# Kernel optimization log

Hardware: AMD Instinct MI355X
Metric: run time of the kernel (lower is better)

## Reference

```python
import jax, jax.numpy as jnp
import numpy as np

IN_C = 256
INTER_C = 64  # in_c // k, k=4
B, H, W = 8, 32, 32
N_TERMS = 5   # numSeriesTerms; numTraceSamples = 1


def setup_inputs():
    key = jax.random.key(0)
    ks = jax.random.split(key, 10)
    s = 0.05
    return {
        "x": jax.random.normal(ks[0], (B, IN_C, H, W), jnp.float32),
        "Wq": jax.random.normal(ks[1], (INTER_C, IN_C), jnp.float32) * s,
        "bq": jax.random.normal(ks[2], (INTER_C,), jnp.float32) * s,
        "Wk": jax.random.normal(ks[3], (INTER_C, IN_C), jnp.float32) * s,
        "bk": jax.random.normal(ks[4], (INTER_C,), jnp.float32) * s,
        "Wc": jax.random.normal(ks[5], (2 * INTER_C,), jnp.float32) * s,
        "Wv": jax.random.normal(ks[6], (IN_C, IN_C), jnp.float32) * s,
        "bv": jax.random.normal(ks[7], (IN_C,), jnp.float32) * s,
        "gamma": jnp.full((1,), 0.5, jnp.float32),
        "u": jax.random.normal(ks[8], (B, IN_C, H, W), jnp.float32),
    }


def _attention(x, Wq, bq, Wk, bk, Wc, Wv, bv, gamma):
    # Attention_concat.forward. concat_conv is a bias-free linear map over the
    # channel concat, so energy[i,j] = <Wc[:ic], q_i> + <Wc[ic:], k_j> exactly.
    b, c, h, w = x.shape
    n = h * w
    xf = x.reshape(b, c, n)                                   # [B,C,N]
    q = jnp.einsum('oc,bcn->bon', Wq, xf) + bq[None, :, None]  # [B,ic,N]
    k = jnp.einsum('oc,bcn->bon', Wk, xf) + bk[None, :, None]  # [B,ic,N]
    ic = Wq.shape[0]
    eq = jnp.einsum('c,bcn->bn', Wc[:ic], q)                  # [B,N]
    ek = jnp.einsum('c,bcn->bn', Wc[ic:], k)                  # [B,N]
    attn = (eq[:, :, None] + ek[:, None, :]) / n              # energy/(H*W), [B,N,N]
    v = jnp.einsum('oc,bcn->bon', Wv, xf) + bv[None, :, None]  # [B,C,N]
    out = jnp.einsum('bcn,bnm->bcm', v, attn).reshape(b, c, h, w)
    return gamma * out + x


def _forward(x, Wq, bq, Wk, bk, Wc, Wv, bv, gamma, u):
    att = lambda z, g: _attention(z, Wq, bq, Wk, bk, Wc, Wv, bv, g)
    # turbulance_hook: runs under torch.no_grad and rescales gamma in-place
    res = att(x, gamma)
    turbu = att(x * 1.0000001, gamma)
    lip = jnp.linalg.norm(turbu - res) / jnp.linalg.norm(x * 1.0000001 - x)
    factor = jax.lax.stop_gradient(jnp.where(lip > 0.9, 0.9 / lip, 1.0))
    gamma_eff = gamma * factor
    Fx, vjp_fn = jax.vjp(lambda z: att(z, gamma_eff), x)
    # power_series_matrix_logarithm_trace: Hutchinson estimate of
    # tr(log(I+J)) ~= sum_j (-1)^{j+1}/j * u^T J^j u, 1 probe, 5 terms
    b = x.shape[0]
    uf = u.reshape(b, -1)
    vcur = u
    tr = jnp.zeros((b,), x.dtype)
    for j in range(1, N_TERMS + 1):
        vcur = vjp_fn(vcur)[0]                 # u^T J^j via repeated vjp
        dot = jnp.sum(vcur.reshape(b, -1) * uf, axis=1)
        tr = tr + ((-1.0) ** (j + 1) / j) * dot
    return x + Fx, tr


def reference(x, Wq, bq, Wk, bk, Wc, Wv, bv, gamma, u):
    return _forward(x, Wq, bq, Wk, bk, Wc, Wv, bv, gamma, u)
```

## Files before the change

kernel.cpp:

```cpp
#include <hip/hip_runtime.h>
#include <math.h>

#define NB 8
#define NC 256
#define NN 1024
#define NICH 64

#define WS_AQ    0
#define WS_AK    256
#define WS_CQ    512
#define WS_CK    513
#define WS_GE    514
#define WS_MOM   520
#define WS_SX    1024
#define WS_XE    3072
#define WS_XK    5120
#define WS_T1P   7424
#define WS_T2P   7488
#define WS_VSU   7680
#define WS_UE    9728
#define WS_VEU   11776
#define WS_CAQ   13824
#define WS_CAK   15872
#define WS_CUAK  17920
#define WS_STAT  20480
#define STAT_STRIDE 2560
#define ST_EQ    0
#define ST_EK    1024
#define ST_SV    2048
#define ST_SVE   2304
#define WS_MAQ   40960
#define WS_MAK   49152
#define WS_EQP   57344
#define WS_EKP   319488
#define WS_MAQP  581632
#define WS_MAKP  843776
#define WS_SX2P  1105920
#define WS_UUP   1106176

__device__ __forceinline__ float dot4(const float4& a, const float4& b) {
    return a.x * b.x + a.y * b.y + a.z * b.z + a.w * b.w;
}
__device__ __forceinline__ float sum4(const float4& a) {
    return a.x + a.y + a.z + a.w;
}

__global__ void k1(const float* __restrict__ x, const float* __restrict__ u,
                   const float* __restrict__ Wq, const float* __restrict__ bq,
                   const float* __restrict__ Wk, const float* __restrict__ bk,
                   const float* __restrict__ Wc, float* __restrict__ ws) {
    const int bid = blockIdx.x;
    const int b = bid >> 5, g = bid & 31;
    const int t = threadIdx.x;
    const int c0 = g * 8;
    const int wid = t >> 6, lane = t & 63;
    __shared__ float aql[8], akl[8];
    __shared__ float sxw[8][4];
    {
        const int c = t >> 5, i = t & 31;
        float a = Wc[i] * Wq[i * NC + c0 + c] + Wc[i + 32] * Wq[(i + 32) * NC + c0 + c];
        float k = Wc[64 + i] * Wk[i * NC + c0 + c] + Wc[96 + i] * Wk[(i + 32) * NC + c0 + c];
        for (int off = 16; off > 0; off >>= 1) {
            a += __shfl_down(a, off, 32);
            k += __shfl_down(k, off, 32);
        }
        if (i == 0) {
            aql[c] = a; akl[c] = k;
            ws[WS_AQ + c0 + c] = a;
            ws[WS_AK + c0 + c] = k;
        }
    }
    if (t < 64) {
        float p = Wc[t] * bq[t], r = Wc[64 + t] * bk[t];
        for (int off = 32; off > 0; off >>= 1) {
            p += __shfl_down(p, off, 64);
            r += __shfl_down(r, off, 64);
        }
        if (t == 0) { ws[WS_CQ] = p; ws[WS_CK] = r; }
    }
    __syncthreads();
    const float4* xb4 = (const float4*)(x + ((size_t)b * NC + c0) * NN);
    const float4* ub4 = (const float4*)(u + ((size_t)b * NC + c0) * NN);
    float4 eqp = {0.f, 0.f, 0.f, 0.f}, ekp = {0.f, 0.f, 0.f, 0.f};
    float4 map = {0.f, 0.f, 0.f, 0.f}, mkp = {0.f, 0.f, 0.f, 0.f};
#pragma unroll
    for (int c = 0; c < 8; ++c) {
        float4 xv = xb4[c * 256 + t];
        float4 uv = ub4[c * 256 + t];
        float a = aql[c], k = akl[c];
        eqp.x += a * xv.x; eqp.y += a * xv.y; eqp.z += a * xv.z; eqp.w += a * xv.w;
        ekp.x += k * xv.x; ekp.y += k * xv.y; ekp.z += k * xv.z; ekp.w += k * xv.w;
        map.x += a * uv.x; map.y += a * uv.y; map.z += a * uv.z; map.w += a * uv.w;
        mkp.x += k * uv.x; mkp.y += k * uv.y; mkp.z += k * uv.z; mkp.w += k * uv.w;
        float xs = sum4(xv);
        for (int off = 32; off > 0; off >>= 1) xs += __shfl_down(xs, off, 64);
        if (lane == 0) sxw[c][wid] = xs;
    }
    __syncthreads();
    if (t < 8) ws[WS_SX + b * NC + c0 + t] = sxw[t][0] + sxw[t][1] + sxw[t][2] + sxw[t][3];
    size_t pb = (size_t)bid * 1024;
    ((float4*)(ws + WS_EQP + pb))[t]  = eqp;
    ((float4*)(ws + WS_EKP + pb))[t]  = ekp;
    ((float4*)(ws + WS_MAQP + pb))[t] = map;
    ((float4*)(ws + WS_MAKP + pb))[t] = mkp;
}

__global__ void k2(float* __restrict__ ws) {
    const int bid = blockIdx.x;
    const int b = bid >> 2, qc = bid & 3;
    const int t = threadIdx.x;
    const int quarter = t >> 6, tn = t & 63;
    const int n4 = qc * 64 + tn;
    __shared__ float4 qb[4][4][64];
    float4 e4 = {0.f, 0.f, 0.f, 0.f}, k4 = {0.f, 0.f, 0.f, 0.f};
    float4 ma4 = {0.f, 0.f, 0.f, 0.f}, mk4 = {0.f, 0.f, 0.f, 0.f};
#pragma unroll
    for (int gg = 0; gg < 8; ++gg) {
        size_t pb = (size_t)(b * 32 + quarter * 8 + gg) * 1024;
        float4 v0 = ((const float4*)(ws + WS_EQP + pb))[n4];
        float4 v1 = ((const float4*)(ws + WS_EKP + pb))[n4];
        float4 v2 = ((const float4*)(ws + WS_MAQP + pb))[n4];
        float4 v3 = ((const float4*)(ws + WS_MAKP + pb))[n4];
        e4.x += v0.x; e4.y += v0.y; e4.z += v0.z; e4.w += v0.w;
        k4.x += v1.x; k4.y += v1.y; k4.z += v1.z; k4.w += v1.w;
        ma4.x += v2.x; ma4.y += v2.y; ma4.z += v2.z; ma4.w += v2.w;
        mk4.x += v3.x; mk4.y += v3.y; mk4.z += v3.z; mk4.w += v3.w;
    }
    qb[0][quarter][tn] = e4; qb[1][quarter][tn] = k4;
    qb[2][quarter][tn] = ma4; qb[3][quarter][tn] = mk4;
    __syncthreads();
    if (t < 64) {
        const float cq = ws[WS_CQ], ck = ws[WS_CK];
        float4 e = qb[0][0][t], kk = qb[1][0][t], ma = qb[2][0][t], mk = qb[3][0][t];
        for (int qq = 1; qq < 4; ++qq) {
            float4 a0 = qb[0][qq][t], a1 = qb[1][qq][t], a2 = qb[2][qq][t], a3 = qb[3][qq][t];
            e.x += a0.x; e.y += a0.y; e.z += a0.z; e.w += a0.w;
            kk.x += a1.x; kk.y += a1.y; kk.z += a1.z; kk.w += a1.w;
            ma.x += a2.x; ma.y += a2.y; ma.z += a2.z; ma.w += a2.w;
            mk.x += a3.x; mk.y += a3.y; mk.z += a3.z; mk.w += a3.w;
        }
        e.x += cq; e.y += cq; e.z += cq; e.w += cq;
        kk.x += ck; kk.y += ck; kk.z += ck; kk.w += ck;
        float* st = ws + WS_STAT + b * STAT_STRIDE;
        ((float4*)(st + ST_EQ))[n4] = e;
        ((float4*)(st + ST_EK))[n4] = kk;
        ((float4*)(ws + WS_MAQ + b * NN))[n4] = ma;
        ((float4*)(ws + WS_MAK + b * NN))[n4] = mk;
        float d0 = sum4(e);
        float d1 = sum4(kk);
        float d2 = dot4(kk, kk);
        float d3 = dot4(e, kk);
        for (int off = 32; off > 0; off >>= 1) {
            d0 += __shfl_down(d0, off, 64);
            d1 += __shfl_down(d1, off, 64);
            d2 += __shfl_down(d2, off, 64);
            d3 += __shfl_down(d3, off, 64);
        }
        if (t == 0) {
            ws[WS_MOM + bid * 4 + 0] = d0;
            ws[WS_MOM + bid * 4 + 1] = d1;
            ws[WS_MOM + bid * 4 + 2] = d2;
            ws[WS_MOM + bid * 4 + 3] = d3;
        }
    }
}

__global__ void k3(const float* __restrict__ x, const float* __restrict__ u,
                   float* __restrict__ ws) {
    const int bid = blockIdx.x;
    const int b = bid >> 5, g = bid & 31;
    const int t = threadIdx.x;
    const int c0 = g * 8;
    const int wid = t >> 6, lane = t & 63;
    __shared__ float wv8[8][8][4];
    __shared__ float accw[2][4];
    const float* st = ws + WS_STAT + b * STAT_STRIDE;
    float4 e4  = ((const float4*)(st + ST_EQ))[t];
    float4 k4v = ((const float4*)(st + ST_EK))[t];
    float4 ma4 = ((const float4*)(ws + WS_MAQ + b * NN))[t];
    float4 mk4 = ((const float4*)(ws + WS_MAK + b * NN))[t];
    const float4* xb4 = (const float4*)(x + ((size_t)b * NC + c0) * NN);
    const float4* ub4 = (const float4*)(u + ((size_t)b * NC + c0) * NN);
    float x2a = 0.f, uua = 0.f;
#pragma unroll
    for (int c = 0; c < 8; ++c) {
        float4 xv = xb4[c * 256 + t];
        float4 uv = ub4[c * 256 + t];
        float d[8];
        d[0] = dot4(xv, e4);
        d[1] = dot4(xv, k4v);
        d[2] = sum4(uv);
        d[3] = dot4(uv, e4);
        d[4] = dot4(uv, k4v);
        d[5] = dot4(xv, ma4);
        d[6] = dot4(xv, mk4);
        d[7] = dot4(uv, mk4);
        x2a += dot4(xv, xv);
        uua += dot4(uv, uv);
        for (int off = 32; off > 0; off >>= 1)
            for (int m = 0; m < 8; ++m) d[m] += __shfl_down(d[m], off, 64);
        if (lane == 0) for (int m = 0; m < 8; ++m) wv8[c][m][wid] = d[m];
    }
    for (int off = 32; off > 0; off >>= 1) {
        x2a += __shfl_down(x2a, off, 64);
        uua += __shfl_down(uua, off, 64);
    }
    if (lane == 0) { accw[0][wid] = x2a; accw[1][wid] = uua; }
    __syncthreads();
    if (t < 8) {
        int c = t;
        float v[8];
        for (int m = 0; m < 8; ++m)
            v[m] = wv8[c][m][0] + wv8[c][m][1] + wv8[c][m][2] + wv8[c][m][3];
        ws[WS_XE   + b * NC + c0 + c] = v[0];
        ws[WS_XK   + b * NC + c0 + c] = v[1];
        ws[WS_VSU  + b * NC + c0 + c] = v[2];
        ws[WS_UE   + b * NC + c0 + c] = v[3];
        ws[WS_VEU  + b * NC + c0 + c] = v[4];
        ws[WS_CAQ  + b * NC + c0 + c] = v[5];
        ws[WS_CAK  + b * NC + c0 + c] = v[6];
        ws[WS_CUAK + b * NC + c0 + c] = v[7];
    }
    if (t == 0) {
        ws[WS_SX2P + bid] = accw[0][0] + accw[0][1] + accw[0][2] + accw[0][3];
        ws[WS_UUP + bid]  = accw[1][0] + accw[1][1] + accw[1][2] + accw[1][3];
    }
}

__global__ void ksv(const float* __restrict__ Wv, const float* __restrict__ bv,
                    float* __restrict__ ws) {
    const int bid = blockIdx.x;
    const int b = bid >> 3, oc = bid & 7;
    const int t = threadIdx.x;
    const int o_sub = t >> 3, ks = t & 7;
    const int o = oc * 32 + o_sub;
    __shared__ float sxl[NC], xel[NC];
    __shared__ float T1s[32], T2s[32];
    sxl[t] = ws[WS_SX + b * NC + t];
    xel[t] = ws[WS_XE + b * NC + t];
    __syncthreads();
    float Seq = 0.f, Sek = 0.f, Sek2 = 0.f;
    for (int q = 0; q < 4; ++q) {
        Seq  += ws[WS_MOM + (b * 4 + q) * 4 + 0];
        Sek  += ws[WS_MOM + (b * 4 + q) * 4 + 1];
        Sek2 += ws[WS_MOM + (b * 4 + q) * 4 + 2];
    }
    const float cq = ws[WS_CQ], ck = ws[WS_CK];
    float wsx = 0.f, wxe = 0.f;
    const float4* wrow = (const float4*)(Wv + (size_t)o * NC);
#pragma unroll
    for (int i = 0; i < 8; ++i) {
        float4 w4 = wrow[i * 8 + ks];
        int k = i * 32 + ks * 4;
        wsx += w4.x * sxl[k] + w4.y * sxl[k + 1] + w4.z * sxl[k + 2] + w4.w * sxl[k + 3];
        wxe += w4.x * xel[k] + w4.y * xel[k + 1] + w4.z * xel[k + 2] + w4.w * xel[k + 3];
    }
    for (int off = 4; off > 0; off >>= 1) {
        wsx += __shfl_down(wsx, off, 8);
        wxe += __shfl_down(wxe, off, 8);
    }
    if (ks == 0) {
        float bvc = bv[o];
        float Sv  = wsx + (float)NN * bvc;
        float SvL = wsx;
        float Sve = wxe + bvc * Seq;
        float* st = ws + WS_STAT + b * STAT_STRIDE;
        st[ST_SV + o] = Sv; st[ST_SVE + o] = Sve;
        float A = 2.f * Sve - bvc * Seq - cq * Sv;
        float sx = sxl[o];
        float xk = ws[WS_XK + b * NC + o];
        float xkL = xk - ck * sx;
        float T1c = A * sx + Sv * xkL + SvL * xk;
        float SP  = Sek - (float)NN * ck;
        float SP2 = Sek2 - 2.f * ck * Sek + (float)NN * ck * ck;
        float SPQ = Sek2 - ck * Sek;
        float T2c = (float)NN * A * A + Sv * Sv * SP2 + SvL * SvL * Sek2
                  + 2.f * A * Sv * SP + 2.f * A * SvL * Sek + 2.f * Sv * SvL * SPQ;
        T1s[o_sub] = T1c; T2s[o_sub] = T2c;
    }
    __syncthreads();
    if (t == 0) {
        float t1 = 0.f, t2 = 0.f;
        for (int i = 0; i < 32; ++i) { t1 += T1s[i]; t2 += T2s[i]; }
        ws[WS_T1P + bid] = t1;
        ws[WS_T2P + bid] = t2;
    }
}

__global__ void kiter(
        const float* __restrict__ Wv, const float* __restrict__ bv,
        const float* __restrict__ gamma, float* __restrict__ ws,
        float* __restrict__ out) {
    const int b = blockIdx.x;
    const int t = threadIdx.x;
    const int o = t & 255, q = t >> 8;
    const int wid4 = o >> 6, lane = t & 63;
    __shared__ unsigned int Wlds[128 * 256];
    __shared__ float VV[2 * NC];
    __shared__ float redPR[2 * 1024];
    __shared__ float dred[9][4];
    __shared__ float gred0[4];
    __shared__ float gredT[2];
    __shared__ float sge;
#pragma unroll 4
    for (int r = 0; r < 32; ++r) {
        int c = r * 8 + q * 2;
        float w0 = Wv[(size_t)c * NC + o];
        float w1 = Wv[(size_t)(c + 1) * NC + o];
        unsigned int b0 = __float_as_uint(w0);
        unsigned int b1 = __float_as_uint(w1);
        b0 = (b0 + 0x7FFFu + ((b0 >> 16) & 1u)) >> 16;
        b1 = (b1 + 0x7FFFu + ((b1 >> 16) & 1u)) & 0xFFFF0000u;
        Wlds[(r * 4 + q) * 256 + o] = b0 | b1;
    }
    {
        float a = 0.f, b1 = 0.f, c1 = 0.f;
        if (t < 256) a = ws[WS_SX2P + t];
        if (t < 64) { b1 = ws[WS_T1P + t]; c1 = ws[WS_T2P + t]; }
        for (int off = 32; off > 0; off >>= 1) {
            a  += __shfl_down(a,  off, 64);
            b1 += __shfl_down(b1, off, 64);
            c1 += __shfl_down(c1, off, 64);
        }
        if (t < 256 && lane == 0) gred0[t >> 6] = a;
        if (t == 0) { gredT[0] = b1; gredT[1] = c1; }
    }
    __syncthreads();
    if (t == 0) {
        float S1 = gred0[0] + gred0[1] + gred0[2] + gred0[3];
        float T1 = gredT[0];
        float T2 = gredT[1];
        float inv = gamma[0] * (1.f / (float)NN);
        float dd = S1 + 2.f * inv * T1 + inv * inv * T2;
        float lip = sqrtf(dd / S1);
        float ge = gamma[0] * ((lip > 0.9f) ? (0.9f / lip) : 1.f);
        sge = ge;
        if (b == 0) ws[WS_GE] = ge;
    }
    __syncthreads();
    const float s = sge * (1.f / (float)NN);
    float Svl_r = 0.f, sxl_r = 0.f, xkl_r = 0.f, caql_r = 0.f, cakl_r = 0.f,
          Uel_r = 0.f, Vsul_r = 0.f, bvl_r = 0.f, aql_r = 0.f, akl_r = 0.f,
          veu_r = 0.f, cuak_r = 0.f, vsreg = 0.f, vereg = 0.f;
    if (t < 256) {
        const float* st = ws + WS_STAT + b * STAT_STRIDE;
        Svl_r  = st[ST_SV + t];
        sxl_r  = ws[WS_SX   + b * NC + t];
        xkl_r  = ws[WS_XK   + b * NC + t];
        caql_r = ws[WS_CAQ  + b * NC + t];
        cakl_r = ws[WS_CAK  + b * NC + t];
        Uel_r  = ws[WS_UE   + b * NC + t];
        Vsul_r = ws[WS_VSU  + b * NC + t];
        veu_r  = ws[WS_VEU  + b * NC + t];
        cuak_r = ws[WS_CUAK + b * NC + t];
        aql_r  = ws[WS_AQ + t];
        akl_r  = ws[WS_AK + t];
        bvl_r  = bv[t];
        vsreg = Vsul_r; vereg = veu_r;
        VV[2 * t] = vsreg; VV[2 * t + 1] = vereg;
    }
    float Seq = 0.f, Sek = 0.f, Sekq = 0.f;
    for (int qq = 0; qq < 4; ++qq) {
        Seq  += ws[WS_MOM + (b * 4 + qq) * 4 + 0];
        Sek  += ws[WS_MOM + (b * 4 + qq) * 4 + 1];
        Sekq += ws[WS_MOM + (b * 4 + qq) * 4 + 3];
    }
    float uu = 0.f;
    for (int g = 0; g < 32; ++g) uu += ws[WS_UUP + b * 32 + g];
    __syncthreads();
    if (t < 256) {
        float d[8] = {Svl_r * cuak_r, aql_r * Vsul_r, akl_r * Vsul_r, akl_r * Uel_r,
                      Svl_r * Vsul_r, Svl_r * veu_r,  Svl_r * aql_r,  Svl_r * akl_r};
        for (int off = 32; off > 0; off >>= 1)
            for (int m = 0; m < 8; ++m) d[m] += __shfl_down(d[m], off, 64);
        if (lane == 0) for (int m = 0; m < 8; ++m) dred[m][wid4] = d[m];
    }
    __syncthreads();
    float g2a = 0.f, aqVsu = 0.f, akVsu = 0.f, akUe = 0.f, SvVsu = 0.f, SvVeu = 0.f,
          Svaq = 0.f, Svak = 0.f;
    if (t < 256) {
        g2a   = dred[0][0] + dred[0][1] + dred[0][2] + dred[0][3];
        aqVsu = dred[1][0] + dred[1][1] + dred[1][2] + dred[1][3];
        akVsu = dred[2][0] + dred[2][1] + dred[2][2] + dred[2][3];
        akUe  = dred[3][0] + dred[3][1] + dred[3][2] + dred[3][3];
        SvVsu = dred[4][0] + dred[4][1] + dred[4][2] + dred[4][3];
        SvVeu = dred[5][0] + dred[5][1] + dred[5][2] + dred[5][3];
        Svaq  = dred[6][0] + dred[6][1] + dred[6][2] + dred[6][3];
        Svak  = dred[7][0] + dred[7][1] + dred[7][2] + dred[7][3];
    }
    __syncthreads();
    const float lam = 1.f + s * Svak;
    float alpha = 1.f, beta = 0.f, gam = 0.f;
    float SxAcc = 0.f, XkAcc = 0.f, CakAcc = 0.f;
    float dot = uu, tr = 0.f;
    const float coef[5] = {1.f, -0.5f, 1.f / 3.f, -0.25f, 0.2f};
    for (int j = 0; j < 5; ++j) {
        float pa = 0.f, ra = 0.f;
#pragma unroll
        for (int ii = 0; ii < 32; ++ii) {
            int i = q * 32 + ii;
            unsigned int w = Wlds[i * 256 + o];
            float4 vv = ((const float4*)VV)[i];
            float wlo = __uint_as_float(w << 16);
            float whi = __uint_as_float(w & 0xFFFF0000u);
            pa += wlo * vv.x + whi * vv.z;
            ra += wlo * vv.y + whi * vv.w;
        }
        redPR[2 * t] = pa; redPR[2 * t + 1] = ra;
        __syncthreads();
        float Pv = 0.f, Rv = 0.f;
        if (t < 256) {
            Pv = s * (redPR[2 * t] + redPR[2 * (t + 256)] + redPR[2 * (t + 512)] + redPR[2 * (t + 768)]);
            Rv = s * (redPR[2 * t + 1] + redPR[2 * (t + 256) + 1] + redPR[2 * (t + 512) + 1] + redPR[2 * (t + 768) + 1]);
            float d[9];
            d[0] = Svl_r * Pv;
            d[1] = Svl_r * Rv;
            d[2] = bvl_r * vsreg;
            d[3] = sxl_r * Pv;
            d[4] = xkl_r * Pv;
            d[5] = caql_r * Pv;
            d[6] = cakl_r * Pv;
            d[7] = Uel_r * Pv;
            d[8] = Vsul_r * Rv;
            for (int off = 32; off > 0; off >>= 1)
                for (int m = 0; m < 9; ++m) d[m] += __shfl_down(d[m], off, 64);
            if (lane == 0) for (int m = 0; m < 9; ++m) dred[m][wid4] = d[m];
        }
        __syncthreads();
        if (t < 256) {
            float sm[9];
            for (int m = 0; m < 9; ++m) sm[m] = dred[m][0] + dred[m][1] + dred[m][2] + dred[m][3];
            const float svP = sm[0], svR = sm[1], bvVs = sm[2], sxP = sm[3], xkP = sm[4],
                        caqP = sm[5], cakP = sm[6], ueP = sm[7], vsuR = sm[8];
            const float sB = s * bvVs;
            float St  = s * (alpha * SvVsu + beta * (float)NN + gam * Seq  + Svaq * SxAcc);
            float tek = s * (alpha * SvVeu + beta * Sek        + gam * Sekq + Svaq * XkAcc);
            float uta = s * (alpha * g2a   + beta * akVsu      + gam * akUe + Svaq * CakAcc);
            dot += ueP + caqP + sB * aqVsu + uta + vsuR;
            tr  += coef[j] * dot;
            float nVs = vsreg + Pv * Seq  + aql_r * (sxP + (float)NN * sB) + akl_r * St  + Rv * (float)NN;
            float nVe = vereg + Pv * Sekq + aql_r * (xkP + sB * Sek)       + akl_r * tek + Rv * Sek;
            vsreg = nVs; vereg = nVe;
            VV[2 * t] = nVs; VV[2 * t + 1] = nVe;
            SxAcc  = lam * SxAcc  + sxP;
            XkAcc  = lam * XkAcc  + xkP;
            CakAcc = lam * CakAcc + cakP;
            beta = lam * beta + Svaq * sB + svR;
            gam  = lam * gam + svP;
            alpha *= lam;
        }
        __syncthreads();
    }
    if (t == 0) out[2097152 + b] = tr;
}

__global__ void kout0(const float* __restrict__ x, const float* __restrict__ ws,
                      float* __restrict__ out) {
    int bid = blockIdx.x;
    int b = bid >> 8, c = bid & 255, t = threadIdx.x;
    float ge = ws[WS_GE] * (1.f / (float)NN);
    const float* st = ws + WS_STAT + b * STAT_STRIDE;
    float sv = st[ST_SV + c], sve = st[ST_SVE + c];
    float4 ek4 = ((const float4*)(st + ST_EK))[t];
    size_t i4 = (size_t)bid * 256 + t;
    float4 x4 = ((const float4*)x)[i4];
    float4 o;
    o.x = 2.f * x4.x + ge * (sve + ek4.x * sv);
    o.y = 2.f * x4.y + ge * (sve + ek4.y * sv);
    o.z = 2.f * x4.z + ge * (sve + ek4.z * sv);
    o.w = 2.f * x4.w + ge * (sve + ek4.w * sv);
    ((float4*)out)[i4] = o;
}

extern "C" void kernel_launch(void* const* d_in, const int* in_sizes, int n_in,
                              void* d_out, int out_size, void* d_ws, size_t ws_size,
                              hipStream_t stream) {
    const float* x     = (const float*)d_in[0];
    const float* Wq    = (const float*)d_in[1];
    const float* bq    = (const float*)d_in[2];
    const float* Wk    = (const float*)d_in[3];
    const float* bk    = (const float*)d_in[4];
    const float* Wc    = (const float*)d_in[5];
    const float* Wv    = (const float*)d_in[6];
    const float* bv    = (const float*)d_in[7];
    const float* gamma = (const float*)d_in[8];
    const float* u     = (const float*)d_in[9];
    float* out = (float*)d_out;
    float* ws  = (float*)d_ws;

    k1   <<<dim3(256),  dim3(256),  0, stream>>>(x, u, Wq, bq, Wk, bk, Wc, ws);
    k2   <<<dim3(32),   dim3(256),  0, stream>>>(ws);
    k3   <<<dim3(256),  dim3(256),  0, stream>>>(x, u, ws);
    ksv  <<<dim3(64),   dim3(256),  0, stream>>>(Wv, bv, ws);
    kiter<<<dim3(8),    dim3(1024), 0, stream>>>(Wv, bv, gamma, ws, out);
    kout0<<<dim3(2048), dim3(256),  0, stream>>>(x, ws, out);
}
```

Baseline: 55.15 us.

## Merge six kernels into four by fusing reductions and the output pass

Kernel k1 is reorganised so each block reduces over 128 channels for a 64-column strip. That makes the partial-sum buffers 16x smaller, and k2 disappears: its final reduction and moment computation move into the start of the old k3 (now kB). The row sums of x are also computed in kB, and the small bias constants are recomputed locally instead of going through workspace. The iterative kernel and the output kernel become one launch, with extra blocks doing the elementwise output. This cuts launch count and workspace traffic, but every output block now redundantly recomputes the lip/gamma reduction.

```diff
diff --git a/kernel.cpp b/kernel.cpp
--- a/kernel.cpp
+++ b/kernel.cpp
@@ -8,10 +8,7 @@
 
 #define WS_AQ    0
 #define WS_AK    256
-#define WS_CQ    512
-#define WS_CK    513
-#define WS_GE    514
-#define WS_MOM   520
+#define WS_MOM2  520
 #define WS_SX    1024
 #define WS_XE    3072
 #define WS_XK    5120
@@ -25,18 +22,15 @@
 #define WS_CUAK  17920
 #define WS_STAT  20480
 #define STAT_STRIDE 2560
-#define ST_EQ    0
 #define ST_EK    1024
 #define ST_SV    2048
 #define ST_SVE   2304
-#define WS_MAQ   40960
-#define WS_MAK   49152
-#define WS_EQP   57344
-#define WS_EKP   319488
-#define WS_MAQP  581632
-#define WS_MAKP  843776
-#define WS_SX2P  1105920
-#define WS_UUP   1106176
+#define WS_EQP2  57344
+#define WS_EKP2  73728
+#define WS_MAQP2 90112
+#define WS_MAKP2 106496
+#define WS_SX2P  123904
+#define WS_UUP   124160
 
 __device__ __forceinline__ float dot4(const float4& a, const float4& b) {
     return a.x * b.x + a.y * b.y + a.z * b.z + a.w * b.w;
@@ -44,141 +38,122 @@
 __device__ __forceinline__ float sum4(const float4& a) {
     return a.x + a.y + a.z + a.w;
 }
-
-__global__ void k1(const float* __restrict__ x, const float* __restrict__ u,
-                   const float* __restrict__ Wq, const float* __restrict__ bq,
-                   const float* __restrict__ Wk, const float* __restrict__ bk,
+__device__ __forceinline__ unsigned int bf16lo(float v) {
+    unsigned int u = __float_as_uint(v);
+    return (u + 0x7FFFu + ((u >> 16) & 1u)) >> 16;
+}
+__device__ __forceinline__ unsigned int bf16hi(float v) {
+    unsigned int u = __float_as_uint(v);
+    return (u + 0x7FFFu + ((u >> 16) & 1u)) & 0xFFFF0000u;
+}
+
+__global__ void kA(const float* __restrict__ x, const float* __restrict__ u,
+                   const float* __restrict__ Wq, const float* __restrict__ Wk,
                    const float* __restrict__ Wc, float* __restrict__ ws) {
     const int bid = blockIdx.x;
+    const int b = bid >> 5, r = bid & 31;
+    const int nq = r >> 1, ch = r & 1;
+    const int t = threadIdx.x;
+    __shared__ float aql[128], akl[128];
+    __shared__ float red[4][4][64];
+    {
+        const int c_local = t >> 1, half = t & 1;
+        const int cg = ch * 128 + c_local;
+        float a = 0.f, k = 0.f;
+#pragma unroll 8
+        for (int i = 0; i < 32; ++i) {
+            int o = half * 32 + i;
+            a += Wc[o] * Wq[o * NC + cg];
+            k += Wc[64 + o] * Wk[o * NC + cg];
+        }
+        a += __shfl_xor(a, 1, 64);
+        k += __shfl_xor(k, 1, 64);
+        if (half == 0) {
+            aql[c_local] = a; akl[c_local] = k;
+            if (nq == 0) { ws[WS_AQ + cg] = a; ws[WS_AK + cg] = k; }
+        }
+    }
+    __syncthreads();
+    const int col = t & 63, grp = t >> 6;
+    const int n = nq * 64 + col;
+    const float* xb = x + ((size_t)b * NC + ch * 128 + grp * 32) * NN + n;
+    const float* ub = u + ((size_t)b * NC + ch * 128 + grp * 32) * NN + n;
+    float eqp = 0.f, ekp = 0.f, map = 0.f, mkp = 0.f;
+#pragma unroll 8
+    for (int i = 0; i < 32; ++i) {
+        float xv = xb[(size_t)i * NN];
+        float uv = ub[(size_t)i * NN];
+        float a = aql[grp * 32 + i], kk = akl[grp * 32 + i];
+        eqp += a * xv; ekp += kk * xv;
+        map += a * uv; mkp += kk * uv;
+    }
+    red[grp][0][col] = eqp; red[grp][1][col] = ekp;
+    red[grp][2][col] = map; red[grp][3][col] = mkp;
+    __syncthreads();
+    if (t < 64) {
+        int idx = (b * 2 + ch) * 1024 + nq * 64 + t;
+        ws[WS_EQP2  + idx] = red[0][0][t] + red[1][0][t] + red[2][0][t] + red[3][0][t];
+        ws[WS_EKP2  + idx] = red[0][1][t] + red[1][1][t] + red[2][1][t] + red[3][1][t];
+        ws[WS_MAQP2 + idx] = red[0][2][t] + red[1][2][t] + red[2][2][t] + red[3][2][t];
+        ws[WS_MAKP2 + idx] = red[0][3][t] + red[1][3][t] + red[2][3][t] + red[3][3][t];
+    }
+}
+
+__global__ void kB(const float* __restrict__ x, const float* __restrict__ u,
+                   const float* __restrict__ Wc, const float* __restrict__ bq,
+                   const float* __restrict__ bk, float* __restrict__ ws) {
+    const int bid = blockIdx.x;
     const int b = bid >> 5, g = bid & 31;
+    const int c0 = g * 8;
     const int t = threadIdx.x;
-    const int c0 = g * 8;
     const int wid = t >> 6, lane = t & 63;
-    __shared__ float aql[8], akl[8];
-    __shared__ float sxw[8][4];
-    {
-        const int c = t >> 5, i = t & 31;
-        float a = Wc[i] * Wq[i * NC + c0 + c] + Wc[i + 32] * Wq[(i + 32) * NC + c0 + c];
-        float k = Wc[64 + i] * Wk[i * NC + c0 + c] + Wc[96 + i] * Wk[(i + 32) * NC + c0 + c];
-        for (int off = 16; off > 0; off >>= 1) {
-            a += __shfl_down(a, off, 32);
-            k += __shfl_down(k, off, 32);
-        }
-        if (i == 0) {
-            aql[c] = a; akl[c] = k;
-            ws[WS_AQ + c0 + c] = a;
-            ws[WS_AK + c0 + c] = k;
-        }
-    }
+    __shared__ float s_cq, s_ck;
+    __shared__ float mred[4][4];
+    __shared__ float wv9[8][9][4];
+    __shared__ float accw[2][4];
     if (t < 64) {
-        float p = Wc[t] * bq[t], r = Wc[64 + t] * bk[t];
+        float p = Wc[t] * bq[t], rr = Wc[64 + t] * bk[t];
         for (int off = 32; off > 0; off >>= 1) {
             p += __shfl_down(p, off, 64);
-            r += __shfl_down(r, off, 64);
-        }
-        if (t == 0) { ws[WS_CQ] = p; ws[WS_CK] = r; }
-    }
-    __syncthreads();
-    const float4* xb4 = (const float4*)(x + ((size_t)b * NC + c0) * NN);
-    const float4* ub4 = (const float4*)(u + ((size_t)b * NC + c0) * NN);
-    float4 eqp = {0.f, 0.f, 0.f, 0.f}, ekp = {0.f, 0.f, 0.f, 0.f};
-    float4 map = {0.f, 0.f, 0.f, 0.f}, mkp = {0.f, 0.f, 0.f, 0.f};
-#pragma unroll
-    for (int c = 0; c < 8; ++c) {
-        float4 xv = xb4[c * 256 + t];
-        float4 uv = ub4[c * 256 + t];
-        float a = aql[c], k = akl[c];
-        eqp.x += a * xv.x; eqp.y += a * xv.y; eqp.z += a * xv.z; eqp.w += a * xv.w;
-        ekp.x += k * xv.x; ekp.y += k * xv.y; ekp.z += k * xv.z; ekp.w += k * xv.w;
-        map.x += a * uv.x; map.y += a * uv.y; map.z += a * uv.z; map.w += a * uv.w;
-        mkp.x += k * uv.x; mkp.y += k * uv.y; mkp.z += k * uv.z; mkp.w += k * uv.w;
-        float xs = sum4(xv);
-        for (int off = 32; off > 0; off >>= 1) xs += __shfl_down(xs, off, 64);
-        if (lane == 0) sxw[c][wid] = xs;
-    }
-    __syncthreads();
-    if (t < 8) ws[WS_SX + b * NC + c0 + t] = sxw[t][0] + sxw[t][1] + sxw[t][2] + sxw[t][3];
-    size_t pb = (size_t)bid * 1024;
-    ((float4*)(ws + WS_EQP + pb))[t]  = eqp;
-    ((float4*)(ws + WS_EKP + pb))[t]  = ekp;
-    ((float4*)(ws + WS_MAQP + pb))[t] = map;
-    ((float4*)(ws + WS_MAKP + pb))[t] = mkp;
-}
-
-__global__ void k2(float* __restrict__ ws) {
-    const int bid = blockIdx.x;
-    const int b = bid >> 2, qc = bid & 3;
-    const int t = threadIdx.x;
-    const int quarter = t >> 6, tn = t & 63;
-    const int n4 = qc * 64 + tn;
-    __shared__ float4 qb[4][4][64];
-    float4 e4 = {0.f, 0.f, 0.f, 0.f}, k4 = {0.f, 0.f, 0.f, 0.f};
-    float4 ma4 = {0.f, 0.f, 0.f, 0.f}, mk4 = {0.f, 0.f, 0.f, 0.f};
-#pragma unroll
-    for (int gg = 0; gg < 8; ++gg) {
-        size_t pb = (size_t)(b * 32 + quarter * 8 + gg) * 1024;
-        float4 v0 = ((const float4*)(ws + WS_EQP + pb))[n4];
-        float4 v1 = ((const float4*)(ws + WS_EKP + pb))[n4];
-        float4 v2 = ((const float4*)(ws + WS_MAQP + pb))[n4];
-        float4 v3 = ((const float4*)(ws + WS_MAKP + pb))[n4];
-        e4.x += v0.x; e4.y += v0.y; e4.z += v0.z; e4.w += v0.w;
-        k4.x += v1.x; k4.y += v1.y; k4.z += v1.z; k4.w += v1.w;
-        ma4.x += v2.x; ma4.y += v2.y; ma4.z += v2.z; ma4.w += v2.w;
-        mk4.x += v3.x; mk4.y += v3.y; mk4.z += v3.z; mk4.w += v3.w;
-    }
-    qb[0][quarter][tn] = e4; qb[1][quarter][tn] = k4;
-    qb[2][quarter][tn] = ma4; qb[3][quarter][tn] = mk4;
-    __syncthreads();
-    if (t < 64) {
-        const float cq = ws[WS_CQ], ck = ws[WS_CK];
-        float4 e = qb[0][0][t], kk = qb[1][0][t], ma = qb[2][0][t], mk = qb[3][0][t];
-        for (int qq = 1; qq < 4; ++qq) {
-            float4 a0 = qb[0][qq][t], a1 = qb[1][qq][t], a2 = qb[2][qq][t], a3 = qb[3][qq][t];
-            e.x += a0.x; e.y += a0.y; e.z += a0.z; e.w += a0.w;
-            kk.x += a1.x; kk.y += a1.y; kk.z += a1.z; kk.w += a1.w;
-            ma.x += a2.x; ma.y += a2.y; ma.z += a2.z; ma.w += a2.w;
-            mk.x += a3.x; mk.y += a3.y; mk.z += a3.z; mk.w += a3.w;
-        }
-        e.x += cq; e.y += cq; e.z += cq; e.w += cq;
-        kk.x += ck; kk.y += ck; kk.z += ck; kk.w += ck;
-        float* st = ws + WS_STAT + b * STAT_STRIDE;
-        ((float4*)(st + ST_EQ))[n4] = e;
-        ((float4*)(st + ST_EK))[n4] = kk;
-        ((float4*)(ws + WS_MAQ + b * NN))[n4] = ma;
-        ((float4*)(ws + WS_MAK + b * NN))[n4] = mk;
-        float d0 = sum4(e);
-        float d1 = sum4(kk);
-        float d2 = dot4(kk, kk);
-        float d3 = dot4(e, kk);
+            rr += __shfl_down(rr, off, 64);
+        }
+        if (t == 0) { s_cq = p; s_ck = rr; }
+    }
+    __syncthreads();
+    const float cq = s_cq, ck = s_ck;
+    float4 e4, k4, ma4, mk4;
+    {
+        float4 a0 = ((const float4*)(ws + WS_EQP2 + (size_t)(b * 2) * 1024))[t];
+        float4 a1 = ((const float4*)(ws + WS_EQP2 + (size_t)(b * 2 + 1) * 1024))[t];
+        e4.x = a0.x + a1.x + cq; e4.y = a0.y + a1.y + cq;
+        e4.z = a0.z + a1.z + cq; e4.w = a0.w + a1.w + cq;
+        a0 = ((const float4*)(ws + WS_EKP2 + (size_t)(b * 2) * 1024))[t];
+        a1 = ((const float4*)(ws + WS_EKP2 + (size_t)(b * 2 + 1) * 1024))[t];
+        k4.x = a0.x + a1.x + ck; k4.y = a0.y + a1.y + ck;
+        k4.z = a0.z + a1.z + ck; k4.w = a0.w + a1.w + ck;
+        a0 = ((const float4*)(ws + WS_MAQP2 + (size_t)(b * 2) * 1024))[t];
+        a1 = ((const float4*)(ws + WS_MAQP2 + (size_t)(b * 2 + 1) * 1024))[t];
+        ma4.x = a0.x + a1.x; ma4.y = a0.y + a1.y; ma4.z = a0.z + a1.z; ma4.w = a0.w + a1.w;
+        a0 = ((const float4*)(ws + WS_MAKP2 + (size_t)(b * 2) * 1024))[t];
+        a1 = ((const float4*)(ws + WS_MAKP2 + (size_t)(b * 2 + 1) * 1024))[t];
+        mk4.x = a0.x + a1.x; mk4.y = a0.y + a1.y; mk4.z = a0.z + a1.z; mk4.w = a0.w + a1.w;
+    }
+    {
+        float d0 = sum4(e4), d1 = sum4(k4), d2 = dot4(k4, k4), d3 = dot4(e4, k4);
         for (int off = 32; off > 0; off >>= 1) {
             d0 += __shfl_down(d0, off, 64);
             d1 += __shfl_down(d1, off, 64);
             d2 += __shfl_down(d2, off, 64);
             d3 += __shfl_down(d3, off, 64);
         }
-        if (t == 0) {
-            ws[WS_MOM + bid * 4 + 0] = d0;
-            ws[WS_MOM + bid * 4 + 1] = d1;
-            ws[WS_MOM + bid * 4 + 2] = d2;
-            ws[WS_MOM + bid * 4 + 3] = d3;
-        }
-    }
-}
-
-__global__ void k3(const float* __restrict__ x, const float* __restrict__ u,
-                   float* __restrict__ ws) {
-    const int bid = blockIdx.x;
-    const int b = bid >> 5, g = bid & 31;
-    const int t = threadIdx.x;
-    const int c0 = g * 8;
-    const int wid = t >> 6, lane = t & 63;
-    __shared__ float wv8[8][8][4];
-    __shared__ float accw[2][4];
-    const float* st = ws + WS_STAT + b * STAT_STRIDE;
-    float4 e4  = ((const float4*)(st + ST_EQ))[t];
-    float4 k4v = ((const float4*)(st + ST_EK))[t];
-    float4 ma4 = ((const float4*)(ws + WS_MAQ + b * NN))[t];
-    float4 mk4 = ((const float4*)(ws + WS_MAK + b * NN))[t];
+        if (lane == 0) { mred[0][wid] = d0; mred[1][wid] = d1; mred[2][wid] = d2; mred[3][wid] = d3; }
+    }
+    __syncthreads();
+    if (t == 0)
+        for (int m = 0; m < 4; ++m)
+            ws[WS_MOM2 + b * 4 + m] = mred[m][0] + mred[m][1] + mred[m][2] + mred[m][3];
+    if (g == 0)
+        ((float4*)(ws + WS_STAT + b * STAT_STRIDE + ST_EK))[t] = k4;
     const float4* xb4 = (const float4*)(x + ((size_t)b * NC + c0) * NN);
     const float4* ub4 = (const float4*)(u + ((size_t)b * NC + c0) * NN);
     float x2a = 0.f, uua = 0.f;
@@ -186,20 +161,21 @@
     for (int c = 0; c < 8; ++c) {
         float4 xv = xb4[c * 256 + t];
         float4 uv = ub4[c * 256 + t];
-        float d[8];
+        float d[9];
         d[0] = dot4(xv, e4);
-        d[1] = dot4(xv, k4v);
+        d[1] = dot4(xv, k4);
         d[2] = sum4(uv);
         d[3] = dot4(uv, e4);
-        d[4] = dot4(uv, k4v);
+        d[4] = dot4(uv, k4);
         d[5] = dot4(xv, ma4);
         d[6] = dot4(xv, mk4);
         d[7] = dot4(uv, mk4);
+        d[8] = sum4(xv);
         x2a += dot4(xv, xv);
         uua += dot4(uv, uv);
         for (int off = 32; off > 0; off >>= 1)
-            for (int m = 0; m < 8; ++m) d[m] += __shfl_down(d[m], off, 64);
-        if (lane == 0) for (int m = 0; m < 8; ++m) wv8[c][m][wid] = d[m];
+            for (int m = 0; m < 9; ++m) d[m] += __shfl_down(d[m], off, 64);
+        if (lane == 0) for (int m = 0; m < 9; ++m) wv9[c][m][wid] = d[m];
     }
     for (int off = 32; off > 0; off >>= 1) {
         x2a += __shfl_down(x2a, off, 64);
@@ -209,9 +185,9 @@
     __syncthreads();
     if (t < 8) {
         int c = t;
-        float v[8];
-        for (int m = 0; m < 8; ++m)
-            v[m] = wv8[c][m][0] + wv8[c][m][1] + wv8[c][m][2] + wv8[c][m][3];
+        float v[9];
+        for (int m = 0; m < 9; ++m)
+            v[m] = wv9[c][m][0] + wv9[c][m][1] + wv9[c][m][2] + wv9[c][m][3];
         ws[WS_XE   + b * NC + c0 + c] = v[0];
         ws[WS_XK   + b * NC + c0 + c] = v[1];
         ws[WS_VSU  + b * NC + c0 + c] = v[2];
@@ -220,6 +196,7 @@
         ws[WS_CAQ  + b * NC + c0 + c] = v[5];
         ws[WS_CAK  + b * NC + c0 + c] = v[6];
         ws[WS_CUAK + b * NC + c0 + c] = v[7];
+        ws[WS_SX   + b * NC + c0 + c] = v[8];
     }
     if (t == 0) {
         ws[WS_SX2P + bid] = accw[0][0] + accw[0][1] + accw[0][2] + accw[0][3];
@@ -228,7 +205,8 @@
 }
 
 __global__ void ksv(const float* __restrict__ Wv, const float* __restrict__ bv,
-                    float* __restrict__ ws) {
+                    const float* __restrict__ Wc, const float* __restrict__ bq,
+                    const float* __restrict__ bk, float* __restrict__ ws) {
     const int bid = blockIdx.x;
     const int b = bid >> 3, oc = bid & 7;
     const int t = threadIdx.x;
@@ -236,16 +214,22 @@
     const int o = oc * 32 + o_sub;
     __shared__ float sxl[NC], xel[NC];
     __shared__ float T1s[32], T2s[32];
+    __shared__ float s_cq, s_ck;
+    if (t < 64) {
+        float p = Wc[t] * bq[t], rr = Wc[64 + t] * bk[t];
+        for (int off = 32; off > 0; off >>= 1) {
+            p += __shfl_down(p, off, 64);
+            rr += __shfl_down(rr, off, 64);
+        }
+        if (t == 0) { s_cq = p; s_ck = rr; }
+    }
     sxl[t] = ws[WS_SX + b * NC + t];
     xel[t] = ws[WS_XE + b * NC + t];
     __syncthreads();
-    float Seq = 0.f, Sek = 0.f, Sek2 = 0.f;
-    for (int q = 0; q < 4; ++q) {
-        Seq  += ws[WS_MOM + (b * 4 + q) * 4 + 0];
-        Sek  += ws[WS_MOM + (b * 4 + q) * 4 + 1];
-        Sek2 += ws[WS_MOM + (b * 4 + q) * 4 + 2];
-    }
-    const float cq = ws[WS_CQ], ck = ws[WS_CK];
+    const float Seq  = ws[WS_MOM2 + b * 4 + 0];
+    const float Sek  = ws[WS_MOM2 + b * 4 + 1];
+    const float Sek2 = ws[WS_MOM2 + b * 4 + 2];
+    const float cq = s_cq, ck = s_ck;
     float wsx = 0.f, wxe = 0.f;
     const float4* wrow = (const float4*)(Wv + (size_t)o * NC);
 #pragma unroll
@@ -287,32 +271,24 @@
     }
 }
 
-__global__ void kiter(
-        const float* __restrict__ Wv, const float* __restrict__ bv,
-        const float* __restrict__ gamma, float* __restrict__ ws,
-        float* __restrict__ out) {
-    const int b = blockIdx.x;
+struct KFSMem {
+    unsigned int Wlds[128 * 256];
+    float VV[512];
+    float redPR[2048];
+    float dred[9][4];
+    float gred0[4];
+    float gredT[2];
+    float sge;
+};
+
+__global__ void kfin(const float* __restrict__ x, const float* __restrict__ Wv,
+                     const float* __restrict__ bv, const float* __restrict__ gamma,
+                     float* __restrict__ ws, float* __restrict__ out) {
+    __shared__ __align__(16) unsigned char smem_raw[sizeof(KFSMem)];
+    KFSMem& S = *(KFSMem*)smem_raw;
+    const int bid = blockIdx.x;
     const int t = threadIdx.x;
-    const int o = t & 255, q = t >> 8;
-    const int wid4 = o >> 6, lane = t & 63;
-    __shared__ unsigned int Wlds[128 * 256];
-    __shared__ float VV[2 * NC];
-    __shared__ float redPR[2 * 1024];
-    __shared__ float dred[9][4];
-    __shared__ float gred0[4];
-    __shared__ float gredT[2];
-    __shared__ float sge;
-#pragma unroll 4
-    for (int r = 0; r < 32; ++r) {
-        int c = r * 8 + q * 2;
-        float w0 = Wv[(size_t)c * NC + o];
-        float w1 = Wv[(size_t)(c + 1) * NC + o];
-        unsigned int b0 = __float_as_uint(w0);
-        unsigned int b1 = __float_as_uint(w1);
-        b0 = (b0 + 0x7FFFu + ((b0 >> 16) & 1u)) >> 16;
-        b1 = (b1 + 0x7FFFu + ((b1 >> 16) & 1u)) & 0xFFFF0000u;
-        Wlds[(r * 4 + q) * 256 + o] = b0 | b1;
-    }
+    const int lane = t & 63;
     {
         float a = 0.f, b1 = 0.f, c1 = 0.f;
         if (t < 256) a = ws[WS_SX2P + t];
@@ -322,23 +298,50 @@
             b1 += __shfl_down(b1, off, 64);
             c1 += __shfl_down(c1, off, 64);
         }
-        if (t < 256 && lane == 0) gred0[t >> 6] = a;
-        if (t == 0) { gredT[0] = b1; gredT[1] = c1; }
+        if (t < 256 && lane == 0) S.gred0[t >> 6] = a;
+        if (t == 0) { S.gredT[0] = b1; S.gredT[1] = c1; }
     }
     __syncthreads();
     if (t == 0) {
-        float S1 = gred0[0] + gred0[1] + gred0[2] + gred0[3];
-        float T1 = gredT[0];
-        float T2 = gredT[1];
+        float S1 = S.gred0[0] + S.gred0[1] + S.gred0[2] + S.gred0[3];
         float inv = gamma[0] * (1.f / (float)NN);
-        float dd = S1 + 2.f * inv * T1 + inv * inv * T2;
+        float dd = S1 + 2.f * inv * S.gredT[0] + inv * inv * S.gredT[1];
         float lip = sqrtf(dd / S1);
-        float ge = gamma[0] * ((lip > 0.9f) ? (0.9f / lip) : 1.f);
-        sge = ge;
-        if (b == 0) ws[WS_GE] = ge;
-    }
-    __syncthreads();
-    const float s = sge * (1.f / (float)NN);
+        S.sge = gamma[0] * ((lip > 0.9f) ? (0.9f / lip) : 1.f);
+    }
+    __syncthreads();
+    const float ge = S.sge;
+
+    if (bid >= 8) {
+        const float gn = ge * (1.f / (float)NN);
+        const int r = t >> 8, tc = t & 255;
+        const int bid2 = (bid - 8) * 4 + r;
+        const int b = bid2 >> 8, c = bid2 & 255;
+        const float* st = ws + WS_STAT + b * STAT_STRIDE;
+        float sv = st[ST_SV + c], sve = st[ST_SVE + c];
+        float4 ek4 = ((const float4*)(st + ST_EK))[tc];
+        size_t i4 = (size_t)bid2 * 256 + tc;
+        float4 x4 = ((const float4*)x)[i4];
+        float4 o;
+        o.x = 2.f * x4.x + gn * (sve + ek4.x * sv);
+        o.y = 2.f * x4.y + gn * (sve + ek4.y * sv);
+        o.z = 2.f * x4.z + gn * (sve + ek4.z * sv);
+        o.w = 2.f * x4.w + gn * (sve + ek4.w * sv);
+        ((float4*)out)[i4] = o;
+        return;
+    }
+
+    const int b = bid;
+    const int o = t & 255, q = t >> 8;
+    const int wid4 = o >> 6;
+#pragma unroll 4
+    for (int r = 0; r < 32; ++r) {
+        int c = r * 8 + q * 2;
+        float w0 = Wv[(size_t)c * NC + o];
+        float w1 = Wv[(size_t)(c + 1) * NC + o];
+        S.Wlds[(r * 4 + q) * 256 + o] = bf16lo(w0) | bf16hi(w1);
+    }
+    const float s = ge * (1.f / (float)NN);
     float Svl_r = 0.f, sxl_r = 0.f, xkl_r = 0.f, caql_r = 0.f, cakl_r = 0.f,
           Uel_r = 0.f, Vsul_r = 0.f, bvl_r = 0.f, aql_r = 0.f, akl_r = 0.f,
           veu_r = 0.f, cuak_r = 0.f, vsreg = 0.f, vereg = 0.f;
@@ -357,14 +360,11 @@
         akl_r  = ws[WS_AK + t];
         bvl_r  = bv[t];
         vsreg = Vsul_r; vereg = veu_r;
-        VV[2 * t] = vsreg; VV[2 * t + 1] = vereg;
-    }
-    float Seq = 0.f, Sek = 0.f, Sekq = 0.f;
-    for (int qq = 0; qq < 4; ++qq) {
-        Seq  += ws[WS_MOM + (b * 4 + qq) * 4 + 0];
-        Sek  += ws[WS_MOM + (b * 4 + qq) * 4 + 1];
-        Sekq += ws[WS_MOM + (b * 4 + qq) * 4 + 3];
-    }
+        S.VV[2 * t] = vsreg; S.VV[2 * t + 1] = vereg;
+    }
+    const float Seq  = ws[WS_MOM2 + b * 4 + 0];
+    const float Sek  = ws[WS_MOM2 + b * 4 + 1];
+    const float Sekq = ws[WS_MOM2 + b * 4 + 3];
     float uu = 0.f;
     for (int g = 0; g < 32; ++g) uu += ws[WS_UUP + b * 32 + g];
     __syncthreads();
@@ -373,20 +373,20 @@
                       Svl_r * Vsul_r, Svl_r * veu_r,  Svl_r * aql_r,  Svl_r * akl_r};
         for (int off = 32; off > 0; off >>= 1)
             for (int m = 0; m < 8; ++m) d[m] += __shfl_down(d[m], off, 64);
-        if (lane == 0) for (int m = 0; m < 8; ++m) dred[m][wid4] = d[m];
+        if (lane == 0) for (int m = 0; m < 8; ++m) S.dred[m][wid4] = d[m];
     }
     __syncthreads();
     float g2a = 0.f, aqVsu = 0.f, akVsu = 0.f, akUe = 0.f, SvVsu = 0.f, SvVeu = 0.f,
           Svaq = 0.f, Svak = 0.f;
     if (t < 256) {
-        g2a   = dred[0][0] + dred[0][1] + dred[0][2] + dred[0][3];
-        aqVsu = dred[1][0] + dred[1][1] + dred[1][2] + dred[1][3];
-        akVsu = dred[2][0] + dred[2][1] + dred[2][2] + dred[2][3];
-        akUe  = dred[3][0] + dred[3][1] + dred[3][2] + dred[3][3];
-        SvVsu = dred[4][0] + dred[4][1] + dred[4][2] + dred[4][3];
-        SvVeu = dred[5][0] + dred[5][1] + dred[5][2] + dred[5][3];
-        Svaq  = dred[6][0] + dred[6][1] + dred[6][2] + dred[6][3];
-        Svak  = dred[7][0] + dred[7][1] + dred[7][2] + dred[7][3];
+        g2a   = S.dred[0][0] + S.dred[0][1] + S.dred[0][2] + S.dred[0][3];
+        aqVsu = S.dred[1][0] + S.dred[1][1] + S.dred[1][2] + S.dred[1][3];
+        akVsu = S.dred[2][0] + S.dred[2][1] + S.dred[2][2] + S.dred[2][3];
+        akUe  = S.dred[3][0] + S.dred[3][1] + S.dred[3][2] + S.dred[3][3];
+        SvVsu = S.dred[4][0] + S.dred[4][1] + S.dred[4][2] + S.dred[4][3];
+        SvVeu = S.dred[5][0] + S.dred[5][1] + S.dred[5][2] + S.dred[5][3];
+        Svaq  = S.dred[6][0] + S.dred[6][1] + S.dred[6][2] + S.dred[6][3];
+        Svak  = S.dred[7][0] + S.dred[7][1] + S.dred[7][2] + S.dred[7][3];
     }
     __syncthreads();
     const float lam = 1.f + s * Svak;
@@ -399,19 +399,18 @@
 #pragma unroll
         for (int ii = 0; ii < 32; ++ii) {
             int i = q * 32 + ii;
-            unsigned int w = Wlds[i * 256 + o];
-            float4 vv = ((const float4*)VV)[i];
+            unsigned int w = S.Wlds[i * 256 + o];
+            float4 vv = ((const float4*)S.VV)[i];
             float wlo = __uint_as_float(w << 16);
             float whi = __uint_as_float(w & 0xFFFF0000u);
             pa += wlo * vv.x + whi * vv.z;
             ra += wlo * vv.y + whi * vv.w;
         }
-        redPR[2 * t] = pa; redPR[2 * t + 1] = ra;
+        S.redPR[2 * t] = pa; S.redPR[2 * t + 1] = ra;
         __syncthreads();
-        float Pv = 0.f, Rv = 0.f;
         if (t < 256) {
-            Pv = s * (redPR[2 * t] + redPR[2 * (t + 256)] + redPR[2 * (t + 512)] + redPR[2 * (t + 768)]);
-            Rv = s * (redPR[2 * t + 1] + redPR[2 * (t + 256) + 1] + redPR[2 * (t + 512) + 1] + redPR[2 * (t + 768) + 1]);
+            float Pv = s * (S.redPR[2 * t] + S.redPR[2 * (t + 256)] + S.redPR[2 * (t + 512)] + S.redPR[2 * (t + 768)]);
+            float Rv = s * (S.redPR[2 * t + 1] + S.redPR[2 * (t + 256) + 1] + S.redPR[2 * (t + 512) + 1] + S.redPR[2 * (t + 768) + 1]);
             float d[9];
             d[0] = Svl_r * Pv;
             d[1] = Svl_r * Rv;
@@ -424,12 +423,11 @@
             d[8] = Vsul_r * Rv;
             for (int off = 32; off > 0; off >>= 1)
                 for (int m = 0; m < 9; ++m) d[m] += __shfl_down(d[m], off, 64);
-            if (lane == 0) for (int m = 0; m < 9; ++m) dred[m][wid4] = d[m];
-        }
-        __syncthreads();
-        if (t < 256) {
+            if (lane == 0) for (int m = 0; m < 9; ++m) S.dred[m][wid4] = d[m];
+            __syncthreads();
             float sm[9];
-            for (int m = 0; m < 9; ++m) sm[m] = dred[m][0] + dred[m][1] + dred[m][2] + dred[m][3];
+            for (int m = 0; m < 9; ++m)
+                sm[m] = S.dred[m][0] + S.dred[m][1] + S.dred[m][2] + S.dred[m][3];
             const float svP = sm[0], svR = sm[1], bvVs = sm[2], sxP = sm[3], xkP = sm[4],
                         caqP = sm[5], cakP = sm[6], ueP = sm[7], vsuR = sm[8];
             const float sB = s * bvVs;
@@ -441,35 +439,19 @@
             float nVs = vsreg + Pv * Seq  + aql_r * (sxP + (float)NN * sB) + akl_r * St  + Rv * (float)NN;
             float nVe = vereg + Pv * Sekq + aql_r * (xkP + sB * Sek)       + akl_r * tek + Rv * Sek;
             vsreg = nVs; vereg = nVe;
-            VV[2 * t] = nVs; VV[2 * t + 1] = nVe;
+            S.VV[2 * t] = nVs; S.VV[2 * t + 1] = nVe;
             SxAcc  = lam * SxAcc  + sxP;
             XkAcc  = lam * XkAcc  + xkP;
             CakAcc = lam * CakAcc + cakP;
             beta = lam * beta + Svaq * sB + svR;
             gam  = lam * gam + svP;
             alpha *= lam;
+        } else {
+            __syncthreads();
         }
         __syncthreads();
     }
     if (t == 0) out[2097152 + b] = tr;
-}
-
-__global__ void kout0(const float* __restrict__ x, const float* __restrict__ ws,
-                      float* __restrict__ out) {
-    int bid = blockIdx.x;
-    int b = bid >> 8, c = bid & 255, t = threadIdx.x;
-    float ge = ws[WS_GE] * (1.f / (float)NN);
-    const float* st = ws + WS_STAT + b * STAT_STRIDE;
-    float sv = st[ST_SV + c], sve = st[ST_SVE + c];
-    float4 ek4 = ((const float4*)(st + ST_EK))[t];
-    size_t i4 = (size_t)bid * 256 + t;
-    float4 x4 = ((const float4*)x)[i4];
-    float4 o;
-    o.x = 2.f * x4.x + ge * (sve + ek4.x * sv);
-    o.y = 2.f * x4.y + ge * (sve + ek4.y * sv);
-    o.z = 2.f * x4.z + ge * (sve + ek4.z * sv);
-    o.w = 2.f * x4.w + ge * (sve + ek4.w * sv);
-    ((float4*)out)[i4] = o;
 }
 
 extern "C" void kernel_launch(void* const* d_in, const int* in_sizes, int n_in,
@@ -488,10 +470,8 @@
     float* out = (float*)d_out;
     float* ws  = (float*)d_ws;
 
-    k1   <<<dim3(256),  dim3(256),  0, stream>>>(x, u, Wq, bq, Wk, bk, Wc, ws);
-    k2   <<<dim3(32),   dim3(256),  0, stream>>>(ws);
-    k3   <<<dim3(256),  dim3(256),  0, stream>>>(x, u, ws);
-    ksv  <<<dim3(64),   dim3(256),  0, stream>>>(Wv, bv, ws);
-    kiter<<<dim3(8),    dim3(1024), 0, stream>>>(Wv, bv, gamma, ws, out);
-    kout0<<<dim3(2048), dim3(256),  0, stream>>>(x, ws, out);
-}
+    kA  <<<dim3(256), dim3(256),  0, stream>>>(x, u, Wq, Wk, Wc, ws);
+    kB  <<<dim3(256), dim3(256),  0, stream>>>(x, u, Wc, bq, bk, ws);
+    ksv <<<dim3(64),  dim3(256),  0, stream>>>(Wv, bv, Wc, bq, bk, ws);
+    kfin<<<dim3(520), dim3(1024), 0, stream>>>(x, Wv, bv, gamma, ws, out);
+}
```

After: 59.42 us. 1.08x slower.
